# Kernel tuning notes

Hardware: AMD Instinct MI355X
Metric: run time of the kernel (lower is better)

The kernel has to match this reference:

```python
import jax, jax.numpy as jnp
import numpy as np

H, D = 4, 32  # num_heads, per-head out dim (out_feats=128)
N_AGENT, N_GT, N_UAV = 50000, 50000, 50000
E = 600000
IN = 64


def _gat(x_src, x_dst, src, dst, W_src, W_dst, al, ar, W_res, b, num_dst):
    """DGL-style bipartite GATConv with residual, bias and ReLU activation."""
    fs = (x_src @ W_src).reshape(-1, H, D)      # [Ns,H,D]
    fd = (x_dst @ W_dst).reshape(-1, H, D)      # [Nd,H,D]
    el = jnp.sum(fs * al, axis=-1)              # [Ns,H]
    er = jnp.sum(fd * ar, axis=-1)              # [Nd,H]
    e = jax.nn.leaky_relu(el[src] + er[dst], 0.2)          # [E,H]
    # segment softmax over incoming edges of each dst node
    emax = jax.ops.segment_max(e, dst, num_segments=num_dst)   # [Nd,H], -inf for deg-0
    ee = jnp.exp(e - emax[dst])
    denom = jax.ops.segment_sum(ee, dst, num_segments=num_dst)
    a = ee / denom[dst]                          # [E,H]
    msg = fs[src] * a[:, :, None]                # [E,H,D]
    rst = jax.ops.segment_sum(msg, dst, num_segments=num_dst)  # [Nd,H,D]; zeros for deg-0
    res = (x_dst @ W_res).reshape(-1, H, D)      # residual projection
    out = jax.nn.relu(rst + res + b.reshape(1, H, D))
    return out.reshape(num_dst, H * D)


def setup_inputs() -> dict:
    key = jax.random.key(0)
    ks = jax.random.split(key, 20)
    s = 0.1  # weight init scale
    return {
        'x_gt': jax.random.normal(ks[0], (N_GT, IN), jnp.float32),
        'x_uav': jax.random.normal(ks[1], (N_UAV, IN), jnp.float32),
        'x_agent': jax.random.normal(ks[2], (N_AGENT, IN), jnp.float32),
        'src_gt': jax.random.randint(ks[3], (E,), 0, N_GT, jnp.int32),
        'dst_gt': jax.random.randint(ks[4], (E,), 0, N_AGENT, jnp.int32),
        'src_uav': jax.random.randint(ks[5], (E,), 0, N_UAV, jnp.int32),
        'dst_uav': jax.random.randint(ks[6], (E,), 0, N_AGENT, jnp.int32),
        'W_src_gt': s * jax.random.normal(ks[7], (IN, H * D), jnp.float32),
        'W_dst_gt': s * jax.random.normal(ks[8], (IN, H * D), jnp.float32),
        'attn_l_gt': s * jax.random.normal(ks[9], (H, D), jnp.float32),
        'attn_r_gt': s * jax.random.normal(ks[10], (H, D), jnp.float32),
        'W_res_gt': s * jax.random.normal(ks[11], (IN, H * D), jnp.float32),
        'b_gt': jnp.zeros((H * D,), jnp.float32),
        'W_src_uav': s * jax.random.normal(ks[12], (IN, H * D), jnp.float32),
        'W_dst_uav': s * jax.random.normal(ks[13], (IN, H * D), jnp.float32),
        'attn_l_uav': s * jax.random.normal(ks[14], (H, D), jnp.float32),
        'attn_r_uav': s * jax.random.normal(ks[15], (H, D), jnp.float32),
        'W_res_uav': s * jax.random.normal(ks[16], (IN, H * D), jnp.float32),
        'b_uav': jnp.zeros((H * D,), jnp.float32),
        'W_f': s * jax.random.normal(ks[17], (2 * H * D, H * D), jnp.float32),
        'b_f': jnp.zeros((H * D,), jnp.float32),
    }


def reference(x_gt, x_uav, x_agent, src_gt, dst_gt, src_uav, dst_uav,
              W_src_gt, W_dst_gt, attn_l_gt, attn_r_gt, W_res_gt, b_gt,
              W_src_uav, W_dst_uav, attn_l_uav, attn_r_uav, W_res_uav, b_uav,
              W_f, b_f):
    h_gt = _gat(x_gt, x_agent, src_gt, dst_gt, W_src_gt, W_dst_gt,
                attn_l_gt, attn_r_gt, W_res_gt, b_gt, N_AGENT)
    h_uav = _gat(x_uav, x_agent, src_uav, dst_uav, W_src_uav, W_dst_uav,
                 attn_l_uav, attn_r_uav, W_res_uav, b_uav, N_AGENT)
    h = jnp.concatenate([h_gt, h_uav], axis=1)   # [N_agent, 256]
    return jax.nn.relu(h @ W_f + b_f)            # [N_agent, 128]
```

## Files before the change

kernel.cpp:

```cpp
#include <hip/hip_runtime.h>
#include <hip/hip_bf16.h>

using bf16 = __hip_bfloat16;

#define NA 50000
#define NE 600000

#define NCH 96
#define CHE 12500
#define HROW 100032
#define PBINS 33344

typedef __attribute__((ext_vector_type(8))) short short8;
typedef __attribute__((ext_vector_type(4))) float f32x4;

#define HBUF_B   0u
#define FS_B     25600000u
#define EL_B     51200000u
#define RECS_B   54400000u
#define HIST_B   68800000u
#define ROW_B    78403072u
#define TOPS_B   78803076u
#define FLAG_B   78803588u
#define WST_GT_B 78803600u
#define WST_UAV_B 78819984u
#define WRT_B    78836368u
#define WFT_B    78869136u
#define ELT_GT_B 78934672u
#define ELT_UAV_B 78936720u
#define ERT_B    78938768u
#define RANK8_B  78940816u
#define WS_BYTES 80140816u

__device__ __forceinline__ float b2f(bf16 v) { return __bfloat162float(v); }

__device__ __forceinline__ float ldf(const void* p, size_t i, int f32) {
    return f32 ? ((const float*)p)[i] : b2f(((const bf16*)p)[i]);
}

__device__ __forceinline__ unsigned short f2bs(float v) {
    bf16 t = __float2bfloat16(v);
    return *(unsigned short*)&t;
}

__device__ __forceinline__ float lrelu_exp(float v) {
    v = v > 0.f ? v : 0.2f * v;
    return __expf(v);
}

__device__ __forceinline__ unsigned int pack_bf16x2(float a, float b) {
    return (unsigned int)f2bs(a) | ((unsigned int)f2bs(b) << 16);
}

__device__ __forceinline__ float lo_f(unsigned int u) { return __uint_as_float(u << 16); }
__device__ __forceinline__ float hi_f(unsigned int u) { return __uint_as_float(u & 0xffff0000u); }

__device__ __forceinline__ float dot2bf(unsigned int a, unsigned int b, float c) {
    float d;
    asm("v_dot2_f32_bf16 %0, %1, %2, %3" : "=v"(d) : "v"(a), "v"(b), "v"(c));
    return d;
}

__device__ __forceinline__ short8 ldfrag8(const void* p, size_t off, int f32) {
    if (!f32) return *(const short8*)((const unsigned short*)p + off);
    union { short8 s; unsigned int u[4]; } r;
    const float* fp = (const float*)p + off;
#pragma unroll
    for (int j = 0; j < 4; ++j) r.u[j] = pack_bf16x2(fp[2 * j], fp[2 * j + 1]);
    return r.s;
}

__device__ int probe_f32(const void* x0) {
    __shared__ int cnt;
    if (threadIdx.x == 0) cnt = 0;
    __syncthreads();
    const bf16* p = (const bf16*)x0;
    int bad = 0;
    for (int i = threadIdx.x; i < 1024; i += 256) {
        float av = fabsf(b2f(p[i]));
        if (!(av <= 1e6f)) bad++;
    }
    if (bad) atomicAdd(&cnt, bad);
    __syncthreads();
    return cnt > 8;
}

__global__ void HeteroVisionConv_29703993819529_kernel(
    const void* x0,
    const void* Wsg, const void* alg, const void* Wdg, const void* arg_,
    const void* Wsu, const void* alu, const void* Wdu, const void* aru,
    const void* Wrg, const void* Wru, const void* Wf,
    unsigned short* wsT_gt, unsigned short* wsT_uav, unsigned short* wrT,
    unsigned short* wfT, unsigned short* elT_gt, unsigned short* elT_uav,
    unsigned short* erT, unsigned int* tops,
    int* flag, unsigned int* outp, long sent) {
    int b = blockIdx.x, t = threadIdx.x;
    int f32 = probe_f32(x0);
    if (b == 20) {
        if (t == 0) { flag[0] = f32; tops[120] = 0u; outp[sent] = 0x447A447Au; }
        return;
    }
    if (b < 8) {
        for (int i = t; i < 32 * 128; i += 256) {
            int k = b * 32 + (i >> 7), n = i & 127;
            wfT[n * 256 + k] = f2bs(ldf(Wf, (size_t)k * 128 + n, f32));
        }
    } else if (b < 12) {
        for (int i = t; i < 16 * 256; i += 256) {
            int k = (b - 8) * 16 + (i >> 8), n = i & 255;
            float v = (n < 128) ? ldf(Wrg, (size_t)k * 128 + n, f32)
                                : ldf(Wru, (size_t)k * 128 + (n - 128), f32);
            wrT[n * 64 + k] = f2bs(v);
        }
    } else if (b < 14) {
        for (int i = t; i < 32 * 128; i += 256) {
            int k = (b - 12) * 32 + (i >> 7), n = i & 127;
            wsT_gt[n * 64 + k] = f2bs(ldf(Wsg, (size_t)k * 128 + n, f32));
        }
    } else if (b < 16) {
        for (int i = t; i < 32 * 128; i += 256) {
            int k = (b - 14) * 32 + (i >> 7), n = i & 127;
            wsT_uav[n * 64 + k] = f2bs(ldf(Wsu, (size_t)k * 128 + n, f32));
        }
    } else {
        int m = b - 16;
        const void* Wm = (m == 0) ? Wsg : (m == 1) ? Wdg : (m == 2) ? Wsu : Wdu;
        const void* Am = (m == 0) ? alg : (m == 1) ? arg_ : (m == 2) ? alu : aru;
        int k = t >> 2, h = t & 3;
        float a = 0.f;
        for (int d = 0; d < 32; ++d)
            a += ldf(Wm, (size_t)k * 128 + h * 32 + d, f32) *
                 ldf(Am, (size_t)h * 32 + d, f32);
        unsigned short v = f2bs(a);
        if (m == 0) {
            elT_gt[h * 64 + k] = v;
            for (int i = t; i < 12 * 64; i += 256) elT_gt[(4 + (i >> 6)) * 64 + (i & 63)] = 0;
        } else if (m == 2) {
            elT_uav[h * 64 + k] = v;
            for (int i = t; i < 12 * 64; i += 256) elT_uav[(4 + (i >> 6)) * 64 + (i & 63)] = 0;
        } else if (m == 1) {
            erT[h * 64 + k] = v;
        } else {
            erT[(4 + h) * 64 + k] = v;
            for (int i = t; i < 8 * 64; i += 256) erT[(8 + (i >> 6)) * 64 + (i & 63)] = 0;
        }
    }
}

__global__ void fused_k(const int* dg, const int* du,
                        unsigned char* hist, unsigned char* rank8,
                        const void* xg, const void* xu, const void* xa,
                        const unsigned short* wsT_gt, const unsigned short* wsT_uav,
                        const unsigned short* elT_gt, const unsigned short* elT_uav,
                        const unsigned short* wrT, const unsigned short* erT,
                        const void* bg, const void* bu,
                        float* elbase, bf16* fs, bf16* hbuf, const int* flag) {
    __shared__ unsigned short Bt[256 * 72];
    __shared__ float bl[256];
    int b = blockIdx.x, t = threadIdx.x;

    if (b < NCH) {
        int c = b;
        int g = c >= 48;
        int eoff = (c - g * 48) * CHE;
        const int* dp = (g ? du : dg) + eoff;
        unsigned char* rk = rank8 + (size_t)g * NE + eoff;
        unsigned int* h32 = (unsigned int*)Bt;
        for (int p = 0; p < 3; ++p) {
            int binLo = p * PBINS;
            unsigned int* out = (unsigned int*)(hist + (size_t)c * HROW + binLo);
            bool live = (binLo + PBINS > g * NA) && (binLo < g * NA + NA);
            if (!live) {
                for (int i = t; i < PBINS / 4; i += 256) out[i] = 0u;
                continue;
            }
            for (int i = t; i < PBINS / 4; i += 256) h32[i] = 0u;
            __syncthreads();
            for (int i = t; i < CHE / 4; i += 256) {
                int4 d4 = *(const int4*)(dp + i * 4);
                int dd[4] = {d4.x, d4.y, d4.z, d4.w};
#pragma unroll
                for (int k = 0; k < 4; ++k) {
                    int rel = g * NA + dd[k] - binLo;
                    if (rel >= 0 && rel < PBINS) {
                        unsigned int sh8 = 8u * (rel & 3);
                        unsigned int old = atomicAdd(&h32[rel >> 2], 1u << sh8);
                        rk[i * 4 + k] = (unsigned char)((old >> sh8) & 255u);
                    }
                }
            }
            __syncthreads();
            for (int i = t; i < PBINS / 4; i += 256) out[i] = h32[i];
            __syncthreads();
        }
        return;
    }
    int nidx = b - NCH;
    int f32 = *flag;
    int lane = t & 63, w = t >> 6;
    int m = lane & 15, quad = lane >> 4;

    if (nidx < 1564) {
        int g = nidx / 782, bb = nidx % 782;
        const void* A = g ? xu : xg;
        const unsigned short* WT = g ? wsT_uav : wsT_gt;
        const unsigned short* ET = g ? elT_uav : elT_gt;
        float* elout = elbase + (g ? 400000 : 0);
        bf16* out = fs + (size_t)g * NA * 128;
        for (int i = t * 8; i < 128 * 64; i += 256 * 8) {
            short8 v = *(const short8*)(WT + i);
            int n = i >> 6, k = i & 63;
            *(short8*)&Bt[n * 72 + k] = v;
        }
        __syncthreads();
        int row = bb * 64 + w * 16 + m;
        int rowc = row < NA ? row : NA - 1;
        short8 a0 = ldfrag8(A, (size_t)rowc * 64 + quad * 8, f32);
        short8 a1 = ldfrag8(A, (size_t)rowc * 64 + 32 + quad * 8, f32);
        f32x4 acc[8];
#pragma unroll
        for (int nt = 0; nt < 8; ++nt) acc[nt] = (f32x4){0.f, 0.f, 0.f, 0.f};
#pragma unroll
        for (int nt = 0; nt < 8; ++nt) {
            short8 b0 = *(const short8*)&Bt[(nt * 16 + m) * 72 + quad * 8];
            short8 b1 = *(const short8*)&Bt[(nt * 16 + m) * 72 + 32 + quad * 8];
            acc[nt] = __builtin_amdgcn_mfma_f32_16x16x32_bf16(a0, b0, acc[nt], 0, 0, 0);
            acc[nt] = __builtin_amdgcn_mfma_f32_16x16x32_bf16(a1, b1, acc[nt], 0, 0, 0);
        }
        f32x4 eacc = (f32x4){0.f, 0.f, 0.f, 0.f};
        {
            short8 e0 = *(const short8*)&ET[m * 64 + quad * 8];
            short8 e1 = *(const short8*)&ET[m * 64 + 32 + quad * 8];
            eacc = __builtin_amdgcn_mfma_f32_16x16x32_bf16(a0, e0, eacc, 0, 0, 0);
            eacc = __builtin_amdgcn_mfma_f32_16x16x32_bf16(a1, e1, eacc, 0, 0, 0);
        }
        int srow = bb * 64 + w * 16 + quad * 4;
#pragma unroll
        for (int nt = 0; nt < 8; ++nt) {
#pragma unroll
            for (int r = 0; r < 4; ++r) {
                int rr = srow + r;
                if (rr < NA) out[(size_t)rr * 128 + nt * 16 + m] = __float2bfloat16(acc[nt][r]);
            }
        }
        if (m < 4) {
#pragma unroll
            for (int r = 0; r < 4; ++r) {
                int rr = srow + r;
                if (rr < NA) elout[(size_t)rr * 4 + m] = eacc[r];
            }
        }
        return;
    }
    int bb = nidx - 1564;
    for (int i = t * 8; i < 256 * 64; i += 256 * 8) {
        short8 v = *(const short8*)(wrT + i);
        int n = i >> 6, k = i & 63;
        *(short8*)&Bt[n * 72 + k] = v;
    }
    bl[t] = (t < 128) ? ldf(bg, t, f32) : ldf(bu, t - 128, f32);
    __syncthreads();
    int row = bb * 64 + w * 16 + m;
    int rowc = row < NA ? row : NA - 1;
    short8 a0 = ldfrag8(xa, (size_t)rowc * 64 + quad * 8, f32);
    short8 a1 = ldfrag8(xa, (size_t)rowc * 64 + 32 + quad * 8, f32);
    f32x4 acc[16];
#pragma unroll
    for (int nt = 0; nt < 16; ++nt) acc[nt] = (f32x4){0.f, 0.f, 0.f, 0.f};
#pragma unroll
    for (int nt = 0; nt < 16; ++nt) {
        short8 b0 = *(const short8*)&Bt[(nt * 16 + m) * 72 + quad * 8];
        short8 b1 = *(const short8*)&Bt[(nt * 16 + m) * 72 + 32 + quad * 8];
        acc[nt] = __builtin_amdgcn_mfma_f32_16x16x32_bf16(a0, b0, acc[nt], 0, 0, 0);
        acc[nt] = __builtin_amdgcn_mfma_f32_16x16x32_bf16(a1, b1, acc[nt], 0, 0, 0);
    }
    f32x4 eacc = (f32x4){0.f, 0.f, 0.f, 0.f};
    {
        short8 e0 = *(const short8*)&erT[m * 64 + quad * 8];
        short8 e1 = *(const short8*)&erT[m * 64 + 32 + quad * 8];
        eacc = __builtin_amdgcn_mfma_f32_16x16x32_bf16(a0, e0, eacc, 0, 0, 0);
        eacc = __builtin_amdgcn_mfma_f32_16x16x32_bf16(a1, e1, eacc, 0, 0, 0);
    }
    int srow = bb * 64 + w * 16 + quad * 4;
#pragma unroll
    for (int nt = 0; nt < 16; ++nt) {
        int col = nt * 16 + m;
#pragma unroll
        for (int r = 0; r < 4; ++r) {
            int rr = srow + r;
            if (rr < NA)
                hbuf[(size_t)rr * 256 + col] = __float2bfloat16(acc[nt][r] + bl[col]);
        }
    }
    if (m < 8) {
        float* ero = (m < 4) ? (elbase + 200000) : (elbase + 600000);
        int mm = m & 3;
#pragma unroll
        for (int r = 0; r < 4; ++r) {
            int rr = srow + r;
            if (rr < NA) ero[(size_t)rr * 4 + mm] = eacc[r];
        }
    }
}

__global__ void scan1_k(unsigned char* hist, unsigned int* row, unsigned int* tops) {
    __shared__ unsigned int sh[256];
    __shared__ int lastf;
    int b = blockIdx.x, t = threadIdx.x;
    int base = b * 1024;
    int off = base + t * 4;
    unsigned int run0 = 0u, run1 = 0u, run2 = 0u, run3 = 0u;
    if (off + 4 <= HROW) {
        for (int c = 0; c < NCH; ++c) {
            unsigned int* hp = (unsigned int*)(hist + (size_t)c * HROW + off);
            unsigned int w = *hp;
            *hp = run0 | (run1 << 8) | (run2 << 16) | (run3 << 24);
            run0 += w & 255u;
            run1 += (w >> 8) & 255u;
            run2 += (w >> 16) & 255u;
            run3 += (w >> 24) & 255u;
        }
    }
    unsigned int v[4];
    v[0] = (base + t * 4 + 0 < 100000) ? run0 : 0u;
    v[1] = (base + t * 4 + 1 < 100000) ? run1 : 0u;
    v[2] = (base + t * 4 + 2 < 100000) ? run2 : 0u;
    v[3] = (base + t * 4 + 3 < 100000) ? run3 : 0u;
    unsigned int s = v[0] + v[1] + v[2] + v[3];
    sh[t] = s;
    __syncthreads();
    for (int o = 1; o < 256; o <<= 1) {
        unsigned int x = (t >= o) ? sh[t - o] : 0u;
        __syncthreads();
        sh[t] += x;
        __syncthreads();
    }
    unsigned int run = sh[t] - s;
    for (int j = 0; j < 4; ++j) {
        if (base + t * 4 + j < 100000) row[base + t * 4 + j] = run;
        run += v[j];
    }
    if (t == 255) tops[b] = sh[255];
    __threadfence();
    __syncthreads();
    if (t == 0) {
        unsigned int tk = atomicAdd(&tops[120], 1u);
        lastf = (tk == 97u);
    }
    __syncthreads();
    if (!lastf) return;
    unsigned int tv = (t < 98) ? __hip_atomic_load(&tops[t], __ATOMIC_RELAXED,
                                                   __HIP_MEMORY_SCOPE_AGENT)
                               : 0u;
    __syncthreads();
    sh[t] = tv;
    __syncthreads();
    for (int o = 1; o < 256; o <<= 1) {
        unsigned int x = (t >= o) ? sh[t - o] : 0u;
        __syncthreads();
        sh[t] += x;
        __syncthreads();
    }
    if (t < 98) tops[t] = sh[t] - tv;
    if (t == 97) row[100000] = tv;
}

__global__ void scatter_k(const int* sg, const int* dg, const int* su, const int* du,
                          const float* elbase, const unsigned int* row,
                          const unsigned int* tops,
                          const unsigned char* hist, const unsigned char* rank8,
                          unsigned int* recs) {
    int q = blockIdx.x * 256 + threadIdx.x;
    if (q >= 2 * NE / 4) return;
    int idx0 = q * 4;
    int g = idx0 >= NE;
    int e0 = idx0 - g * NE;
    int4 s4 = *(const int4*)((g ? su : sg) + e0);
    int4 d4 = *(const int4*)((g ? du : dg) + e0);
    uchar4 r4 = *(const uchar4*)(rank8 + (size_t)idx0);
    int c = g * 48 + e0 / CHE;
    const float4* el4 = (const float4*)(elbase + (g ? 400000 : 0));
    const float4* er4 = (const float4*)(elbase + (g ? 600000 : 200000));
    const unsigned char* ch = hist + (size_t)c * HROW + g * NA;
    int ss[4] = {s4.x, s4.y, s4.z, s4.w};
    int dd[4] = {d4.x, d4.y, d4.z, d4.w};
    unsigned int lr[4] = {r4.x, r4.y, r4.z, r4.w};
    unsigned int cb[4], ro[4], tp[4];
    float4 l[4], r[4];
#pragma unroll
    for (int k = 0; k < 4; ++k) {
        int bin = g * NA + dd[k];
        cb[k] = ch[dd[k]];
        ro[k] = row[bin];
        tp[k] = tops[bin >> 10];
        l[k] = el4[ss[k]];
        r[k] = er4[dd[k]];
    }
#pragma unroll
    for (int k = 0; k < 4; ++k) {
        unsigned int pos = ro[k] + tp[k] + cb[k] + lr[k];
        uint3 rec;
        rec.x = (unsigned int)ss[k];
        rec.y = pack_bf16x2(lrelu_exp(l[k].x + r[k].x), lrelu_exp(l[k].y + r[k].y));
        rec.z = pack_bf16x2(lrelu_exp(l[k].z + r[k].z), lrelu_exp(l[k].w + r[k].w));
        *(uint3*)(recs + (size_t)pos * 3) = rec;
    }
}

__global__ void gather_k(const unsigned int* row, const unsigned int* tops,
                         const unsigned int* recs,
                         const bf16* fs, bf16* hbuf) {
    int wid = (blockIdx.x * 256 + threadIdx.x) >> 6;
    int lane = threadIdx.x & 63;
    if (wid >= 2 * NA) return;
    int g = wid / NA, d = wid - g * NA;
    int bin = g * NA + d;
    int eg = lane >> 4;
    int cl = lane & 15;
    int hsel = cl >> 3;
    unsigned int shl = ((cl >> 2) & 1) ? 0u : 16u;
    unsigned int start = row[bin] + tops[bin >> 10];
    unsigned int end   = row[bin + 1] + tops[(bin + 1) >> 10];
    const uint4* fs4 = (const uint4*)(fs + (size_t)g * NA * 128);
    uint4* hp = (uint4*)(hbuf + (size_t)d * 256 + g * 128) + cl;
    uint4 rv;
    if (lane < 16) rv = *hp;

    float denom = 0.f;
    float a[8];
#pragma unroll
    for (int k = 0; k < 8; ++k) a[k] = 0.f;

    if (start < end) {
        uint3 rr[4], rn[4];
        uint4 uu[4];
#pragma unroll
        for (int j = 0; j < 4; ++j) {
            unsigned int idx = start + 4 * j + eg;
            rr[j] = *(const uint3*)(recs + (size_t)(idx < end ? idx : end - 1) * 3);
        }
#pragma unroll
        for (int j = 0; j < 4; ++j)
            uu[j] = fs4[(size_t)rr[j].x * 16 + cl];
#pragma unroll
        for (int j = 0; j < 4; ++j) {
            unsigned int idx = start + 16 + 4 * j + eg;
            rn[j] = *(const uint3*)(recs + (size_t)(idx < end ? idx : end - 1) * 3);
        }
        for (unsigned int i = start; i < end; i += 16) {
            uint4 un[4];
            uint3 rnn[4];
#pragma unroll
            for (int j = 0; j < 4; ++j)
                un[j] = fs4[(size_t)rn[j].x * 16 + cl];
#pragma unroll
            for (int j = 0; j < 4; ++j) {
                unsigned int idx = i + 32 + 4 * j + eg;
                rnn[j] = *(const uint3*)(recs + (size_t)(idx < end ? idx : end - 1) * 3);
            }
#pragma unroll
            for (int p = 0; p < 2; ++p) {
                int j0 = 2 * p, j1 = 2 * p + 1;
                unsigned int pp0 = hsel ? rr[j0].z : rr[j0].y;
                unsigned int pp1 = hsel ? rr[j1].z : rr[j1].y;
                pp0 <<= shl;
                pp1 <<= shl;
                if (i + 4 * j0 + eg >= end) pp0 = 0u;
                if (i + 4 * j1 + eg >= end) pp1 = 0u;
                unsigned int w01 = __builtin_amdgcn_perm(pp1, pp0, 0x07060302u);
                denom = dot2bf(w01, 0x3F803F80u, denom);
                const unsigned int* u0 = (const unsigned int*)&uu[j0];
                const unsigned int* u1 = (const unsigned int*)&uu[j1];
#pragma unroll
                for (int w2 = 0; w2 < 4; ++w2) {
                    unsigned int lop = __builtin_amdgcn_perm(u1[w2], u0[w2], 0x05040100u);
                    unsigned int hip = __builtin_amdgcn_perm(u1[w2], u0[w2], 0x07060302u);
                    a[2 * w2]     = dot2bf(lop, w01, a[2 * w2]);
                    a[2 * w2 + 1] = dot2bf(hip, w01, a[2 * w2 + 1]);
                }
            }
#pragma unroll
            for (int j = 0; j < 4; ++j) { rr[j] = rn[j]; rn[j] = rnn[j]; uu[j] = un[j]; }
        }
    }
#pragma unroll
    for (int k = 0; k < 8; ++k) {
        a[k] += __shfl_xor(a[k], 16, 64);
        a[k] += __shfl_xor(a[k], 32, 64);
    }
    denom += __shfl_xor(denom, 16, 64);
    denom += __shfl_xor(denom, 32, 64);
    if (lane < 16) {
        float inv = (end > start) ? 1.f / denom : 0.f;
        float v0 = a[0] * inv + lo_f(rv.x);
        float v1 = a[1] * inv + hi_f(rv.x);
        float v2 = a[2] * inv + lo_f(rv.y);
        float v3 = a[3] * inv + hi_f(rv.y);
        float v4 = a[4] * inv + lo_f(rv.z);
        float v5 = a[5] * inv + hi_f(rv.z);
        float v6 = a[6] * inv + lo_f(rv.w);
        float v7 = a[7] * inv + hi_f(rv.w);
        v0 = v0 > 0.f ? v0 : 0.f;
        v1 = v1 > 0.f ? v1 : 0.f;
        v2 = v2 > 0.f ? v2 : 0.f;
        v3 = v3 > 0.f ? v3 : 0.f;
        v4 = v4 > 0.f ? v4 : 0.f;
        v5 = v5 > 0.f ? v5 : 0.f;
        v6 = v6 > 0.f ? v6 : 0.f;
        v7 = v7 > 0.f ? v7 : 0.f;
        uint4 o;
        o.x = pack_bf16x2(v0, v1);
        o.y = pack_bf16x2(v2, v3);
        o.z = pack_bf16x2(v4, v5);
        o.w = pack_bf16x2(v6, v7);
        *hp = o;
    }
}

__global__ void final_k(const bf16* hbuf, const unsigned short* wfT,
                        const void* bfp, void* outp, const int* flag) {
    int f32 = *flag;
    int b = blockIdx.x;
    __shared__ unsigned short Bt[128 * 72];
    __shared__ float bl[128];
    int t = threadIdx.x;
    if (t < 128) bl[t] = ldf(bfp, t, f32);
    int lane = t & 63, w = t >> 6;
    int m = lane & 15, quad = lane >> 4;
    int row = b * 64 + w * 16 + m;
    int rowc = row < NA ? row : NA - 1;
    f32x4 acc[8];
#pragma unroll
    for (int nt = 0; nt < 8; ++nt) acc[nt] = (f32x4){0.f, 0.f, 0.f, 0.f};
    for (int kc = 0; kc < 4; ++kc) {
        __syncthreads();
        for (int i = t * 8; i < 128 * 64; i += 256 * 8) {
            int n = i >> 6, k = i & 63;
            short8 v = *(const short8*)(wfT + (size_t)n * 256 + kc * 64 + k);
            *(short8*)&Bt[n * 72 + k] = v;
        }
        __syncthreads();
        short8 a0 = *(const short8*)((const unsigned short*)hbuf +
                                     (size_t)rowc * 256 + kc * 64 + quad * 8);
        short8 a1 = *(const short8*)((const unsigned short*)hbuf +
                                     (size_t)rowc * 256 + kc * 64 + 32 + quad * 8);
#pragma unroll
        for (int nt = 0; nt < 8; ++nt) {
            short8 b0 = *(const short8*)&Bt[(nt * 16 + m) * 72 + quad * 8];
            short8 b1 = *(const short8*)&Bt[(nt * 16 + m) * 72 + 32 + quad * 8];
            acc[nt] = __builtin_amdgcn_mfma_f32_16x16x32_bf16(a0, b0, acc[nt], 0, 0, 0);
            acc[nt] = __builtin_amdgcn_mfma_f32_16x16x32_bf16(a1, b1, acc[nt], 0, 0, 0);
        }
    }
    int srow = b * 64 + w * 16 + quad * 4;
#pragma unroll
    for (int nt = 0; nt < 8; ++nt) {
        int col = nt * 16 + m;
        float bv = bl[col];
#pragma unroll
        for (int r = 0; r < 4; ++r) {
            int rr = srow + r;
            if (rr < NA) {
                float v = acc[nt][r] + bv;
                v = v > 0.f ? v : 0.f;
                if (f32) ((float*)outp)[(size_t)rr * 128 + col] = v;
                else ((bf16*)outp)[(size_t)rr * 128 + col] = __float2bfloat16(v);
            }
        }
    }
}

extern "C" void kernel_launch(void* const* d_in, const int* in_sizes, int n_in,
                              void* d_out, int out_size, void* d_ws, size_t ws_size,
                              hipStream_t stream) {
    const void* x_gt     = d_in[0];
    const void* x_uav    = d_in[1];
    const void* x_ag     = d_in[2];
    const int*  src_gt   = (const int*)d_in[3];
    const int*  dst_gt   = (const int*)d_in[4];
    const int*  src_uav  = (const int*)d_in[5];
    const int*  dst_uav  = (const int*)d_in[6];
    const void* Wsrc_gt  = d_in[7];
    const void* Wdst_gt  = d_in[8];
    const void* al_gt    = d_in[9];
    const void* ar_gt    = d_in[10];
    const void* Wres_gt  = d_in[11];
    const void* b_gt     = d_in[12];
    const void* Wsrc_uav = d_in[13];
    const void* Wdst_uav = d_in[14];
    const void* al_uav   = d_in[15];
    const void* ar_uav   = d_in[16];
    const void* Wres_uav = d_in[17];
    const void* b_uav    = d_in[18];
    const void* W_f      = d_in[19];
    const void* b_f      = d_in[20];

    char* wsb = (char*)d_ws;
    bf16* hbuf = (bf16*)(wsb + HBUF_B);
    bf16* fs = (bf16*)(wsb + FS_B);
    float* el = (float*)(wsb + EL_B);
    unsigned int* recs = (unsigned int*)(wsb + RECS_B);
    unsigned char* hist = (unsigned char*)(wsb + HIST_B);
    unsigned int* row = (unsigned int*)(wsb + ROW_B);
    unsigned int* tops = (unsigned int*)(wsb + TOPS_B);
    int* flag = (int*)(wsb + FLAG_B);
    unsigned short* wsT_gt = (unsigned short*)(wsb + WST_GT_B);
    unsigned short* wsT_uav = (unsigned short*)(wsb + WST_UAV_B);
    unsigned short* wrT = (unsigned short*)(wsb + WRT_B);
    unsigned short* wfT = (unsigned short*)(wsb + WFT_B);
    unsigned short* elT_gt = (unsigned short*)(wsb + ELT_GT_B);
    unsigned short* elT_uav = (unsigned short*)(wsb + ELT_UAV_B);
    unsigned short* erT = (unsigned short*)(wsb + ERT_B);
    unsigned char* rank8 = (unsigned char*)(wsb + RANK8_B);

    if (ws_size < (size_t)WS_BYTES) {
        hipMemsetAsync(d_out, 0x42, (size_t)out_size * 2, stream);
        return;
    }

    long sent = (long)out_size / 2 - 1;

    HeteroVisionConv_29703993819529_kernel<<<21, 256, 0, stream>>>(
        x_gt, Wsrc_gt, al_gt, Wdst_gt, ar_gt, Wsrc_uav, al_uav, Wdst_uav, ar_uav,
        Wres_gt, Wres_uav, W_f,
        wsT_gt, wsT_uav, wrT, wfT, elT_gt, elT_uav, erT, tops,
        flag, (unsigned int*)d_out, sent);
    fused_k<<<NCH + 2346, 256, 0, stream>>>(dst_gt, dst_uav, hist, rank8,
                                            x_gt, x_uav, x_ag,
                                            wsT_gt, wsT_uav, elT_gt, elT_uav,
                                            wrT, erT, b_gt, b_uav,
                                            el, fs, hbuf, flag);
    scan1_k<<<98, 256, 0, stream>>>(hist, row, tops);
    scatter_k<<<1172, 256, 0, stream>>>(src_gt, dst_gt, src_uav, dst_uav,
                                        el, row, tops, hist, rank8, recs);
    gather_k<<<25000, 256, 0, stream>>>(row, tops, recs, fs, hbuf);
    final_k<<<782, 256, 0, stream>>>(hbuf, wfT, b_f, d_out, flag);
}
```

Measured before the change: 280.4 us.

## Process four destination nodes per wave in gather with cross-node prefetch

The gather kernel now assigns four consecutive destination nodes to each wavefront instead of one, and launches a quarter as many blocks. Edge records and source-feature rows for the next node are prefetched while the current node is accumulated, so load latency is hidden across node boundaries rather than only within one node's edge list. Each node averages about 12 edges, so the old per-wave prologue and tail were a large share of the work. In exchange there are fewer waves to hide latency, more register pressure from the extra prefetch buffers, and a simpler un-pipelined loop for nodes with more than 16 edges.

```diff
diff --git a/kernel.cpp b/kernel.cpp
--- a/kernel.cpp
+++ b/kernel.cpp
@@ -407,113 +407,138 @@
     }
 }
 
+__device__ __forceinline__ uint3 ldrec(const unsigned int* recs, unsigned int s,
+                                       unsigned int e, unsigned int slot) {
+    unsigned int idx = s + slot;
+    unsigned int c = (s < e) ? (idx < e ? idx : e - 1) : 0u;
+    return *(const uint3*)(recs + (size_t)c * 3);
+}
+
+__device__ __forceinline__ void gacc16(unsigned int rbase, unsigned int e,
+                                       const uint3* rr, const uint4* uu,
+                                       int hsel, unsigned int shl, int eg,
+                                       float& denom, float* a) {
+#pragma unroll
+    for (int p = 0; p < 2; ++p) {
+        int j0 = 2 * p, j1 = 2 * p + 1;
+        unsigned int pp0 = hsel ? rr[j0].z : rr[j0].y;
+        unsigned int pp1 = hsel ? rr[j1].z : rr[j1].y;
+        pp0 <<= shl;
+        pp1 <<= shl;
+        if (rbase + 4 * j0 + eg >= e) pp0 = 0u;
+        if (rbase + 4 * j1 + eg >= e) pp1 = 0u;
+        unsigned int w01 = __builtin_amdgcn_perm(pp1, pp0, 0x07060302u);
+        denom = dot2bf(w01, 0x3F803F80u, denom);
+        const unsigned int* u0 = (const unsigned int*)&uu[j0];
+        const unsigned int* u1 = (const unsigned int*)&uu[j1];
+#pragma unroll
+        for (int w2 = 0; w2 < 4; ++w2) {
+            unsigned int lop = __builtin_amdgcn_perm(u1[w2], u0[w2], 0x05040100u);
+            unsigned int hip = __builtin_amdgcn_perm(u1[w2], u0[w2], 0x07060302u);
+            a[2 * w2]     = dot2bf(lop, w01, a[2 * w2]);
+            a[2 * w2 + 1] = dot2bf(hip, w01, a[2 * w2 + 1]);
+        }
+    }
+}
+
 __global__ void gather_k(const unsigned int* row, const unsigned int* tops,
                          const unsigned int* recs,
                          const bf16* fs, bf16* hbuf) {
-    int wid = (blockIdx.x * 256 + threadIdx.x) >> 6;
+    int wv = (blockIdx.x * 256 + threadIdx.x) >> 6;
     int lane = threadIdx.x & 63;
-    if (wid >= 2 * NA) return;
-    int g = wid / NA, d = wid - g * NA;
-    int bin = g * NA + d;
+    if (wv >= 25000) return;
+    int g = wv / 12500;
+    int d0 = (wv - g * 12500) * 4;
+    int bin0 = g * NA + d0;
     int eg = lane >> 4;
     int cl = lane & 15;
     int hsel = cl >> 3;
     unsigned int shl = ((cl >> 2) & 1) ? 0u : 16u;
-    unsigned int start = row[bin] + tops[bin >> 10];
-    unsigned int end   = row[bin + 1] + tops[(bin + 1) >> 10];
+    unsigned int st[5];
+#pragma unroll
+    for (int i = 0; i < 5; ++i) st[i] = row[bin0 + i] + tops[(bin0 + i) >> 10];
     const uint4* fs4 = (const uint4*)(fs + (size_t)g * NA * 128);
-    uint4* hp = (uint4*)(hbuf + (size_t)d * 256 + g * 128) + cl;
-    uint4 rv;
-    if (lane < 16) rv = *hp;
-
-    float denom = 0.f;
-    float a[8];
-#pragma unroll
-    for (int k = 0; k < 8; ++k) a[k] = 0.f;
-
-    if (start < end) {
-        uint3 rr[4], rn[4];
-        uint4 uu[4];
-#pragma unroll
-        for (int j = 0; j < 4; ++j) {
-            unsigned int idx = start + 4 * j + eg;
-            rr[j] = *(const uint3*)(recs + (size_t)(idx < end ? idx : end - 1) * 3);
-        }
-#pragma unroll
-        for (int j = 0; j < 4; ++j)
-            uu[j] = fs4[(size_t)rr[j].x * 16 + cl];
-#pragma unroll
-        for (int j = 0; j < 4; ++j) {
-            unsigned int idx = start + 16 + 4 * j + eg;
-            rn[j] = *(const uint3*)(recs + (size_t)(idx < end ? idx : end - 1) * 3);
-        }
-        for (unsigned int i = start; i < end; i += 16) {
-            uint4 un[4];
-            uint3 rnn[4];
-#pragma unroll
-            for (int j = 0; j < 4; ++j)
-                un[j] = fs4[(size_t)rn[j].x * 16 + cl];
-#pragma unroll
-            for (int j = 0; j < 4; ++j) {
-                unsigned int idx = i + 32 + 4 * j + eg;
-                rnn[j] = *(const uint3*)(recs + (size_t)(idx < end ? idx : end - 1) * 3);
+    uint4 rv[4];
+    if (lane < 16) {
+#pragma unroll
+        for (int i = 0; i < 4; ++i)
+            rv[i] = *((uint4*)(hbuf + (size_t)(d0 + i) * 256 + g * 128) + cl);
+    }
+
+    uint3 rA[4], rB[4], rC[4];
+    uint4 uA[4], uB[4];
+#pragma unroll
+    for (int j = 0; j < 4; ++j) rA[j] = ldrec(recs, st[0], st[1], 4 * j + eg);
+#pragma unroll
+    for (int j = 0; j < 4; ++j) uA[j] = fs4[(size_t)rA[j].x * 16 + cl];
+#pragma unroll
+    for (int j = 0; j < 4; ++j) rB[j] = ldrec(recs, st[1], st[2], 4 * j + eg);
+
+#pragma unroll
+    for (int i = 0; i < 4; ++i) {
+        unsigned int s = st[i], e = st[i + 1];
+        if (i < 3) {
+#pragma unroll
+            for (int j = 0; j < 4; ++j) uB[j] = fs4[(size_t)rB[j].x * 16 + cl];
+        }
+        if (i < 2) {
+#pragma unroll
+            for (int j = 0; j < 4; ++j) rC[j] = ldrec(recs, st[i + 2], st[i + 3], 4 * j + eg);
+        }
+        float denom = 0.f;
+        float a[8];
+#pragma unroll
+        for (int k = 0; k < 8; ++k) a[k] = 0.f;
+        if (s < e) {
+            gacc16(s, e, rA, uA, hsel, shl, eg, denom, a);
+            for (unsigned int ii = s + 16; ii < e; ii += 16) {
+                uint3 rT[4];
+                uint4 uT[4];
+#pragma unroll
+                for (int j = 0; j < 4; ++j) {
+                    unsigned int idx = ii + 4 * j + eg;
+                    rT[j] = *(const uint3*)(recs + (size_t)(idx < e ? idx : e - 1) * 3);
+                }
+#pragma unroll
+                for (int j = 0; j < 4; ++j) uT[j] = fs4[(size_t)rT[j].x * 16 + cl];
+                gacc16(ii, e, rT, uT, hsel, shl, eg, denom, a);
             }
-#pragma unroll
-            for (int p = 0; p < 2; ++p) {
-                int j0 = 2 * p, j1 = 2 * p + 1;
-                unsigned int pp0 = hsel ? rr[j0].z : rr[j0].y;
-                unsigned int pp1 = hsel ? rr[j1].z : rr[j1].y;
-                pp0 <<= shl;
-                pp1 <<= shl;
-                if (i + 4 * j0 + eg >= end) pp0 = 0u;
-                if (i + 4 * j1 + eg >= end) pp1 = 0u;
-                unsigned int w01 = __builtin_amdgcn_perm(pp1, pp0, 0x07060302u);
-                denom = dot2bf(w01, 0x3F803F80u, denom);
-                const unsigned int* u0 = (const unsigned int*)&uu[j0];
-                const unsigned int* u1 = (const unsigned int*)&uu[j1];
-#pragma unroll
-                for (int w2 = 0; w2 < 4; ++w2) {
-                    unsigned int lop = __builtin_amdgcn_perm(u1[w2], u0[w2], 0x05040100u);
-                    unsigned int hip = __builtin_amdgcn_perm(u1[w2], u0[w2], 0x07060302u);
-                    a[2 * w2]     = dot2bf(lop, w01, a[2 * w2]);
-                    a[2 * w2 + 1] = dot2bf(hip, w01, a[2 * w2 + 1]);
-                }
-            }
-#pragma unroll
-            for (int j = 0; j < 4; ++j) { rr[j] = rn[j]; rn[j] = rnn[j]; uu[j] = un[j]; }
-        }
-    }
-#pragma unroll
-    for (int k = 0; k < 8; ++k) {
-        a[k] += __shfl_xor(a[k], 16, 64);
-        a[k] += __shfl_xor(a[k], 32, 64);
-    }
-    denom += __shfl_xor(denom, 16, 64);
-    denom += __shfl_xor(denom, 32, 64);
-    if (lane < 16) {
-        float inv = (end > start) ? 1.f / denom : 0.f;
-        float v0 = a[0] * inv + lo_f(rv.x);
-        float v1 = a[1] * inv + hi_f(rv.x);
-        float v2 = a[2] * inv + lo_f(rv.y);
-        float v3 = a[3] * inv + hi_f(rv.y);
-        float v4 = a[4] * inv + lo_f(rv.z);
-        float v5 = a[5] * inv + hi_f(rv.z);
-        float v6 = a[6] * inv + lo_f(rv.w);
-        float v7 = a[7] * inv + hi_f(rv.w);
-        v0 = v0 > 0.f ? v0 : 0.f;
-        v1 = v1 > 0.f ? v1 : 0.f;
-        v2 = v2 > 0.f ? v2 : 0.f;
-        v3 = v3 > 0.f ? v3 : 0.f;
-        v4 = v4 > 0.f ? v4 : 0.f;
-        v5 = v5 > 0.f ? v5 : 0.f;
-        v6 = v6 > 0.f ? v6 : 0.f;
-        v7 = v7 > 0.f ? v7 : 0.f;
-        uint4 o;
-        o.x = pack_bf16x2(v0, v1);
-        o.y = pack_bf16x2(v2, v3);
-        o.z = pack_bf16x2(v4, v5);
-        o.w = pack_bf16x2(v6, v7);
-        *hp = o;
+        }
+#pragma unroll
+        for (int k = 0; k < 8; ++k) {
+            a[k] += __shfl_xor(a[k], 16, 64);
+            a[k] += __shfl_xor(a[k], 32, 64);
+        }
+        denom += __shfl_xor(denom, 16, 64);
+        denom += __shfl_xor(denom, 32, 64);
+        if (lane < 16) {
+            float inv = (e > s) ? 1.f / denom : 0.f;
+            uint4* hp = (uint4*)(hbuf + (size_t)(d0 + i) * 256 + g * 128) + cl;
+            float v0 = a[0] * inv + lo_f(rv[i].x);
+            float v1 = a[1] * inv + hi_f(rv[i].x);
+            float v2 = a[2] * inv + lo_f(rv[i].y);
+            float v3 = a[3] * inv + hi_f(rv[i].y);
+            float v4 = a[4] * inv + lo_f(rv[i].z);
+            float v5 = a[5] * inv + hi_f(rv[i].z);
+            float v6 = a[6] * inv + lo_f(rv[i].w);
+            float v7 = a[7] * inv + hi_f(rv[i].w);
+            v0 = v0 > 0.f ? v0 : 0.f;
+            v1 = v1 > 0.f ? v1 : 0.f;
+            v2 = v2 > 0.f ? v2 : 0.f;
+            v3 = v3 > 0.f ? v3 : 0.f;
+            v4 = v4 > 0.f ? v4 : 0.f;
+            v5 = v5 > 0.f ? v5 : 0.f;
+            v6 = v6 > 0.f ? v6 : 0.f;
+            v7 = v7 > 0.f ? v7 : 0.f;
+            uint4 o;
+            o.x = pack_bf16x2(v0, v1);
+            o.y = pack_bf16x2(v2, v3);
+            o.z = pack_bf16x2(v4, v5);
+            o.w = pack_bf16x2(v6, v7);
+            *hp = o;
+        }
+#pragma unroll
+        for (int j = 0; j < 4; ++j) { rA[j] = rB[j]; uA[j] = uB[j]; rB[j] = rC[j]; }
     }
 }
 
@@ -633,6 +658,6 @@
     scan1_k<<<98, 256, 0, stream>>>(hist, row, tops);
     scatter_k<<<1172, 256, 0, stream>>>(src_gt, dst_gt, src_uav, dst_uav,
                                         el, row, tops, hist, rank8, recs);
-    gather_k<<<25000, 256, 0, stream>>>(row, tops, recs, fs, hbuf);
+    gather_k<<<6250, 256, 0, stream>>>(row, tops, recs, fs, hbuf);
     final_k<<<782, 256, 0, stream>>>(hbuf, wfT, b_f, d_out, flag);
 }
```

Result: no change. 284.7 us (+1.5%).
